# Kernel tuning notes

Hardware: AMD Instinct MI355X
Metric: run time of the kernel (lower is better)

Reference implementation:

```python
import jax, jax.numpy as jnp
import numpy as np

N_NODES = 100000
N_EDGES = 1600000
N_FEAT = 500
N_CLASSES = 40


def gcn_conv(x, W, b, src, dst, n):
    """PyG GCNConv: add self-loops, symmetric deg normalization, linear + bias."""
    h = x @ W                                   # [n, out]
    loop = jnp.arange(n, dtype=src.dtype)
    s = jnp.concatenate([src, loop])            # sources incl. self-loops
    d = jnp.concatenate([dst, loop])            # destinations incl. self-loops
    deg = jax.ops.segment_sum(jnp.ones_like(d, dtype=x.dtype), d, num_segments=n)
    dinv = jax.lax.rsqrt(deg)                   # deg >= 1 because of self-loops
    norm = dinv[s] * dinv[d]                    # [E+n]
    out = jax.ops.segment_sum(h[s] * norm[:, None], d, num_segments=n)
    return out + b


def glorot(key, fan_in, fan_out):
    lim = np.sqrt(6.0 / (fan_in + fan_out)).astype(np.float32)
    return jax.random.uniform(key, (fan_in, fan_out), jnp.float32, -lim, lim)


def setup_inputs() -> dict:
    key = jax.random.key(0)
    ks = jax.random.split(key, 6)
    x = jax.random.normal(ks[0], (N_NODES, N_FEAT), dtype=jnp.float32)
    edge_index = jax.random.randint(ks[1], (2, N_EDGES), 0, N_NODES, dtype=jnp.int64)
    return {
        "x": x,
        "edge_index": edge_index,
        "W1": glorot(ks[2], N_FEAT, 128), "b1": jnp.zeros((128,), jnp.float32),
        "W2": glorot(ks[3], 128, 64),     "b2": jnp.zeros((64,), jnp.float32),
        "W4": glorot(ks[4], 64, N_CLASSES), "b4": jnp.zeros((N_CLASSES,), jnp.float32),
    }


def reference(x, edge_index, W1, b1, W2, b2, W4, b4):
    src, dst = edge_index[0], edge_index[1]
    n = x.shape[0]
    h = jax.nn.relu(gcn_conv(x, W1, b1, src, dst, n))
    h = jax.nn.relu(gcn_conv(h, W2, b2, src, dst, n))
    h = gcn_conv(h, W4, b4, src, dst, n)
    return jax.nn.log_softmax(h, axis=1)
```

## Files before the change

kernel.cpp:

```cpp
#include <hip/hip_runtime.h>
#include <hip/hip_bf16.h>
#include <cmath>

#define NNODES 100000
#define NEDGES 1600000
#define SCAN_B 1024

typedef __attribute__((ext_vector_type(8))) short bf16x8;
typedef __attribute__((ext_vector_type(4))) float f32x4;

__device__ __forceinline__ unsigned short f2bf(float f) {
    unsigned u = __builtin_bit_cast(unsigned, f);
    unsigned r = (u + 0x7fffu + ((u >> 16) & 1u)) >> 16;
    return (unsigned short)r;
}
__device__ __forceinline__ float bflo(unsigned v) {
    return __builtin_bit_cast(float, v << 16);
}
__device__ __forceinline__ float bfhi(unsigned v) {
    return __builtin_bit_cast(float, v & 0xffff0000u);
}


__global__ void zero_deg(int* __restrict__ deg, int n) {
    int i = blockIdx.x * 256 + threadIdx.x;
    if (i < n) deg[i] = 0;
}

__global__ __launch_bounds__(256) void count_deg_xcd(const int* __restrict__ dst,
                                                     int* __restrict__ deg, int E) {
    int g = blockIdx.x & 7;
    int sub = blockIdx.x >> 3;
    int nsub = gridDim.x >> 3;
    int lo = g * (NNODES / 8), hi = lo + (NNODES / 8);
    for (int e = sub * 256 + threadIdx.x; e < E; e += nsub * 256) {
        int d = dst[e];
        if (d >= lo && d < hi) atomicAdd(&deg[d], 1);
    }
}

__global__ void calc_dinv(const int* __restrict__ deg, float* __restrict__ dinv, int n) {
    int i = blockIdx.x * 256 + threadIdx.x;
    if (i < n) dinv[i] = rsqrtf(1.0f + (float)deg[i]);
}

__global__ __launch_bounds__(SCAN_B) void scan_block(const int* __restrict__ deg,
                                                     int* __restrict__ pos,
                                                     int* __restrict__ bsums, int n) {
    __shared__ int s[SCAN_B];
    int tid = threadIdx.x;
    int gid = blockIdx.x * SCAN_B + tid;
    int v = (gid < n) ? deg[gid] : 0;
    s[tid] = v;
    __syncthreads();
    for (int off = 1; off < SCAN_B; off <<= 1) {
        int t = (tid >= off) ? s[tid - off] : 0;
        __syncthreads();
        s[tid] += t;
        __syncthreads();
    }
    if (gid < n) pos[gid] = s[tid] - v;
    if (tid == SCAN_B - 1) bsums[blockIdx.x] = s[tid];
}

__global__ __launch_bounds__(128) void scan_sums(int* __restrict__ bsums, int nb) {
    __shared__ int s[128];
    int tid = threadIdx.x;
    int v = (tid < nb) ? bsums[tid] : 0;
    s[tid] = v;
    __syncthreads();
    for (int off = 1; off < 128; off <<= 1) {
        int t = (tid >= off) ? s[tid - off] : 0;
        __syncthreads();
        s[tid] += t;
        __syncthreads();
    }
    if (tid < nb) bsums[tid] = s[tid] - v;
}

__global__ __launch_bounds__(SCAN_B) void add_off(int* __restrict__ pos,
                                                  const int* __restrict__ bsums, int n) {
    int gid = blockIdx.x * SCAN_B + threadIdx.x;
    if (gid < n) pos[gid] += bsums[blockIdx.x];
}

__global__ __launch_bounds__(256) void csr_fill_xcd(const int* __restrict__ src,
                                                    const int* __restrict__ dst,
                                                    int* __restrict__ pos,
                                                    int* __restrict__ csr_src, int E) {
    int g = blockIdx.x & 7;
    int sub = blockIdx.x >> 3;
    int nsub = gridDim.x >> 3;
    int lo = g * (NNODES / 8), hi = lo + (NNODES / 8);
    for (int e = sub * 256 + threadIdx.x; e < E; e += nsub * 256) {
        int d = dst[e];
        if (d >= lo && d < hi) {
            int slot = atomicAdd(&pos[d], 1);
            csr_src[slot] = src[e];
        }
    }
}


__global__ __launch_bounds__(256) void conv_w1f(const float* __restrict__ W1,
                                                unsigned short* __restrict__ W1f) {
    int idx = blockIdx.x * 256 + threadIdx.x;
    if (idx >= 8192) return;
    int t = idx >> 9;
    int rest = idx & 511;
    int j = rest >> 6;
    int l = rest & 63;
    int n = j * 16 + (l & 15);
    int kb = t * 32 + (l >> 4) * 8;
    bf16x8 o;
    #pragma unroll
    for (int jj = 0; jj < 8; jj++) {
        int k = kb + jj;
        o[jj] = (k < 500) ? (short)f2bf(W1[k * 128 + n]) : (short)0;
    }
    *(bf16x8*)(W1f + (size_t)idx * 8) = o;
}

__global__ __launch_bounds__(256) void conv_w2f(const float* __restrict__ W2,
                                                unsigned short* __restrict__ W2f) {
    int idx = blockIdx.x * 256 + threadIdx.x;
    if (idx >= 1024) return;
    int t = idx >> 8;
    int rest = idx & 255;
    int j = rest >> 6;
    int l = rest & 63;
    int n = j * 16 + (l & 15);
    int kb = t * 32 + (l >> 4) * 8;
    bf16x8 o;
    #pragma unroll
    for (int jj = 0; jj < 8; jj++)
        o[jj] = (short)f2bf(W2[(kb + jj) * 64 + n]);
    *(bf16x8*)(W2f + (size_t)idx * 8) = o;
}


__global__ __launch_bounds__(256) void gemm1_mfma(
    const float* __restrict__ x, const unsigned short* __restrict__ W1f,
    const float* __restrict__ dinv, unsigned short* __restrict__ C, int M)
{
    const int tid = threadIdx.x;
    const int w = tid >> 6;
    const int l = tid & 63;
    const int lm = l & 15;
    const int q = l >> 4;
    const int row0 = blockIdx.x * 128;

    const float* abase[2];
    #pragma unroll
    for (int i = 0; i < 2; i++) {
        int r = row0 + w * 32 + i * 16 + lm;
        if (r >= M) r = M - 1;
        abase[i] = x + (size_t)r * 500 + q * 8;
    }

    f32x4 acc[2][8];
    #pragma unroll
    for (int i = 0; i < 2; i++)
        #pragma unroll
        for (int j = 0; j < 8; j++) acc[i][j] = (f32x4){0.f, 0.f, 0.f, 0.f};

    for (int t = 0; t < 16; ++t) {
        const int k0 = t * 32;
        bf16x8 af[2];
        if (k0 + q * 8 + 8 <= 500) {
            #pragma unroll
            for (int i = 0; i < 2; i++) {
                float4 u = *(const float4*)(abase[i] + k0);
                float4 v = *(const float4*)(abase[i] + k0 + 4);
                bf16x8 o;
                o[0] = f2bf(u.x); o[1] = f2bf(u.y); o[2] = f2bf(u.z); o[3] = f2bf(u.w);
                o[4] = f2bf(v.x); o[5] = f2bf(v.y); o[6] = f2bf(v.z); o[7] = f2bf(v.w);
                af[i] = o;
            }
        } else {
            #pragma unroll
            for (int i = 0; i < 2; i++) {
                bf16x8 o;
                #pragma unroll
                for (int jj = 0; jj < 8; jj++) {
                    int k = k0 + q * 8 + jj;
                    o[jj] = (k < 500) ? (short)f2bf(abase[i][k0 + jj]) : (short)0;
                }
                af[i] = o;
            }
        }
        bf16x8 bfr[8];
        #pragma unroll
        for (int j = 0; j < 8; j++)
            bfr[j] = *(const bf16x8*)(W1f + (((size_t)t * 8 + j) * 64 + l) * 8);
        #pragma unroll
        for (int i = 0; i < 2; i++)
            #pragma unroll
            for (int j = 0; j < 8; j++)
                acc[i][j] = __builtin_amdgcn_mfma_f32_16x16x32_bf16(af[i], bfr[j], acc[i][j], 0, 0, 0);
    }

    #pragma unroll
    for (int i = 0; i < 2; i++) {
        #pragma unroll
        for (int reg = 0; reg < 4; reg++) {
            int grow = row0 + w * 32 + i * 16 + q * 4 + reg;
            if (grow < M) {
                float d = dinv[grow];
                #pragma unroll
                for (int j = 0; j < 8; j++)
                    C[(size_t)grow * 128 + j * 16 + lm] = f2bf(d * acc[i][j][reg]);
            }
        }
    }
}


__global__ __launch_bounds__(256) void gemm2_mfma(
    const unsigned short* __restrict__ A, const unsigned short* __restrict__ W2f,
    const float* __restrict__ dinv, unsigned short* __restrict__ C, int M)
{
    const int tid = threadIdx.x;
    const int w = tid >> 6;
    const int l = tid & 63;
    const int lm = l & 15;
    const int q = l >> 4;
    const int row0 = blockIdx.x * 128;

    const unsigned short* abase[2];
    #pragma unroll
    for (int i = 0; i < 2; i++) {
        int r = row0 + w * 32 + i * 16 + lm;
        if (r >= M) r = M - 1;
        abase[i] = A + (size_t)r * 128 + q * 8;
    }

    f32x4 acc[2][4];
    #pragma unroll
    for (int i = 0; i < 2; i++)
        #pragma unroll
        for (int j = 0; j < 4; j++) acc[i][j] = (f32x4){0.f, 0.f, 0.f, 0.f};

    for (int t = 0; t < 4; ++t) {
        const int k0 = t * 32;
        bf16x8 af[2];
        #pragma unroll
        for (int i = 0; i < 2; i++)
            af[i] = *(const bf16x8*)(abase[i] + k0);
        bf16x8 bfr[4];
        #pragma unroll
        for (int j = 0; j < 4; j++)
            bfr[j] = *(const bf16x8*)(W2f + (((size_t)t * 4 + j) * 64 + l) * 8);
        #pragma unroll
        for (int i = 0; i < 2; i++)
            #pragma unroll
            for (int j = 0; j < 4; j++)
                acc[i][j] = __builtin_amdgcn_mfma_f32_16x16x32_bf16(af[i], bfr[j], acc[i][j], 0, 0, 0);
    }

    #pragma unroll
    for (int i = 0; i < 2; i++) {
        #pragma unroll
        for (int reg = 0; reg < 4; reg++) {
            int grow = row0 + w * 32 + i * 16 + q * 4 + reg;
            if (grow < M) {
                float d = dinv[grow];
                #pragma unroll
                for (int j = 0; j < 4; j++)
                    C[(size_t)grow * 64 + j * 16 + lm] = f2bf(d * acc[i][j][reg]);
            }
        }
    }
}


__global__ __launch_bounds__(256) void gemm_n40(
    const float* __restrict__ A, const float* __restrict__ W,
    const float* __restrict__ bias, const float* __restrict__ dinv,
    float* __restrict__ C, int M)
{
    __shared__ float sA[32][65];
    __shared__ float sW[64][40];
    const int row0 = blockIdx.x * 32;
    for (int idx = threadIdx.x; idx < 64 * 40; idx += 256)
        sW[idx / 40][idx % 40] = W[idx];
    for (int idx = threadIdx.x; idx < 32 * 64; idx += 256) {
        int r = idx >> 6, k = idx & 63;
        int row = row0 + r;
        float v = 0.0f;
        if (row < M) v = fmaxf(A[(long)row * 64 + k] + bias[k], 0.0f);
        sA[r][k] = v;
    }
    __syncthreads();
    float acc[5] = {0, 0, 0, 0, 0};
    int rr[5], cc[5];
    #pragma unroll
    for (int j = 0; j < 5; j++) {
        int o = threadIdx.x + 256 * j;
        rr[j] = o / 40; cc[j] = o % 40;
    }
    for (int k = 0; k < 64; k++) {
        #pragma unroll
        for (int j = 0; j < 5; j++) acc[j] += sA[rr[j]][k] * sW[k][cc[j]];
    }
    #pragma unroll
    for (int j = 0; j < 5; j++) {
        int row = row0 + rr[j];
        if (row < M) C[(long)row * 40 + cc[j]] = dinv[row] * acc[j];
    }
}


template<int F, bool OBF16>
__global__ __launch_bounds__(256) void gather_bf(
    const unsigned short* __restrict__ h, const float* __restrict__ dinv,
    const int* __restrict__ pos, const int* __restrict__ csr_src,
    void* __restrict__ outv, const float* __restrict__ bias, int n)
{
    constexpr int P = F / 2;
    unsigned t = blockIdx.x * 256u + threadIdx.x;
    unsigned node = t / P;
    unsigned p = t - node * P;
    if (node >= (unsigned)n) return;
    int e0 = node ? pos[node - 1] : 0;
    int e1 = pos[node];
    float di = dinv[node];
    unsigned sv = *(const unsigned*)(h + (size_t)node * F + 2 * p);
    float a0 = bflo(sv);
    float a1 = bfhi(sv);
    int j = e0;
    for (; j + 4 <= e1; j += 4) {
        int s0 = csr_src[j], s1 = csr_src[j + 1], s2 = csr_src[j + 2], s3 = csr_src[j + 3];
        unsigned v0 = *(const unsigned*)(h + (size_t)s0 * F + 2 * p);
        unsigned v1 = *(const unsigned*)(h + (size_t)s1 * F + 2 * p);
        unsigned v2 = *(const unsigned*)(h + (size_t)s2 * F + 2 * p);
        unsigned v3 = *(const unsigned*)(h + (size_t)s3 * F + 2 * p);
        a0 += bflo(v0) + bflo(v1) + bflo(v2) + bflo(v3);
        a1 += bfhi(v0) + bfhi(v1) + bfhi(v2) + bfhi(v3);
    }
    for (; j < e1; j++) {
        int s = csr_src[j];
        unsigned v = *(const unsigned*)(h + (size_t)s * F + 2 * p);
        a0 += bflo(v);
        a1 += bfhi(v);
    }
    a0 *= di; a1 *= di;
    if constexpr (OBF16) {
        a0 = fmaxf(a0 + bias[2 * p], 0.0f);
        a1 = fmaxf(a1 + bias[2 * p + 1], 0.0f);
        ((unsigned*)outv)[(size_t)node * P + p] =
            ((unsigned)f2bf(a1) << 16) | (unsigned)f2bf(a0);
    } else {
        float2 r; r.x = a0; r.y = a1;
        ((float2*)outv)[(size_t)node * P + p] = r;
    }
}


template<int F>
__global__ __launch_bounds__(256) void gather_agg(
    const float* __restrict__ h, const float* __restrict__ dinv,
    const int* __restrict__ pos, const int* __restrict__ csr_src,
    float* __restrict__ out, int n)
{
    unsigned t = blockIdx.x * 256u + threadIdx.x;
    unsigned node = t / F;
    unsigned c = t - node * F;
    if (node >= (unsigned)n) return;
    int e0 = node ? pos[node - 1] : 0;
    int e1 = pos[node];
    float di = dinv[node];
    float acc = h[(size_t)node * F + c];
    int j = e0;
    for (; j + 4 <= e1; j += 4) {
        int s0 = csr_src[j], s1 = csr_src[j + 1], s2 = csr_src[j + 2], s3 = csr_src[j + 3];
        float v0 = h[(size_t)s0 * F + c];
        float v1 = h[(size_t)s1 * F + c];
        float v2 = h[(size_t)s2 * F + c];
        float v3 = h[(size_t)s3 * F + c];
        acc += v0 + v1 + v2 + v3;
    }
    for (; j < e1; j++) {
        int s = csr_src[j];
        acc += h[(size_t)s * F + c];
    }
    out[(size_t)node * F + c] = di * acc;
}


__global__ __launch_bounds__(256) void logsoftmax40(const float* __restrict__ h,
                                                    const float* __restrict__ bias,
                                                    float* __restrict__ out, int n) {
    int wave = (blockIdx.x * 256 + threadIdx.x) >> 6;
    int lane = threadIdx.x & 63;
    if (wave >= n) return;
    float x = 0.0f, v = -INFINITY;
    if (lane < 40) { x = h[(long)wave * 40 + lane] + bias[lane]; v = x; }
    #pragma unroll
    for (int off = 32; off; off >>= 1) v = fmaxf(v, __shfl_xor(v, off, 64));
    float ex = (lane < 40) ? expf(x - v) : 0.0f;
    float s = ex;
    #pragma unroll
    for (int off = 32; off; off >>= 1) s += __shfl_xor(s, off, 64);
    if (lane < 40) out[(long)wave * 40 + lane] = x - v - logf(s);
}


extern "C" void kernel_launch(void* const* d_in, const int* in_sizes, int n_in,
                              void* d_out, int out_size, void* d_ws, size_t ws_size,
                              hipStream_t stream) {
    const float* x  = (const float*)d_in[0];
    const int*   ei = (const int*)d_in[1];
    const float* W1 = (const float*)d_in[2];
    const float* b1 = (const float*)d_in[3];
    const float* W2 = (const float*)d_in[4];
    const float* b2 = (const float*)d_in[5];
    const float* W4 = (const float*)d_in[6];
    const float* b4 = (const float*)d_in[7];
    float* out = (float*)d_out;
    float* ws  = (float*)d_ws;

    const int N = NNODES, E = NEDGES;
    const int* src = ei;
    const int* dst = ei + E;

    float*          dinv    = ws;
    int*            deg     = (int*)(ws + 100000);
    int*            pos     = (int*)(ws + 200000);
    int*            bsums   = (int*)(ws + 300000);
    int*            csr_src = (int*)(ws + 300200);
    unsigned short* W1f     = (unsigned short*)(ws + 1900200);
    unsigned short* W2f     = (unsigned short*)(ws + 1933000);
    unsigned short* h1      = (unsigned short*)(ws + 1937100);
    unsigned short* h2      = (unsigned short*)(ws + 1937100);
    unsigned short* a1      = (unsigned short*)(ws + 8337100);
    float*          h3      = ws + 8337100;
    float*          a2      = ws + 14737100;
    float*          a3      = out;

    const int nscan = (N + SCAN_B - 1) / SCAN_B;

    zero_deg<<<(N + 255) / 256, 256, 0, stream>>>(deg, N);
    count_deg_xcd<<<1024, 256, 0, stream>>>(dst, deg, E);
    calc_dinv<<<(N + 255) / 256, 256, 0, stream>>>(deg, dinv, N);
    scan_block<<<nscan, SCAN_B, 0, stream>>>(deg, pos, bsums, N);
    scan_sums<<<1, 128, 0, stream>>>(bsums, nscan);
    add_off<<<nscan, SCAN_B, 0, stream>>>(pos, bsums, N);
    csr_fill_xcd<<<1024, 256, 0, stream>>>(src, dst, pos, csr_src, E);

    conv_w1f<<<32, 256, 0, stream>>>(W1, W1f);
    conv_w2f<<<4, 256, 0, stream>>>(W2, W2f);

    gemm1_mfma<<<(N + 127) / 128, 256, 0, stream>>>(x, W1f, dinv, h1, N);
    {
        unsigned tot = (unsigned)N * 64u;
        gather_bf<128, true><<<(tot + 255) / 256, 256, 0, stream>>>(h1, dinv, pos, csr_src, a1, b1, N);
    }

    gemm2_mfma<<<(N + 127) / 128, 256, 0, stream>>>(a1, W2f, dinv, h2, N);
    {
        unsigned tot = (unsigned)N * 32u;
        gather_bf<64, false><<<(tot + 255) / 256, 256, 0, stream>>>(h2, dinv, pos, csr_src, a2, nullptr, N);
    }

    gemm_n40<<<(N + 31) / 32, 256, 0, stream>>>(a2, W4, b2, dinv, h3, N);
    {
        unsigned tot = (unsigned)N * 40u;
        gather_agg<40><<<(tot + 255) / 256, 256, 0, stream>>>(h3, dinv, pos, csr_src, a3, N);
    }

    logsoftmax40<<<(N * 64 + 255) / 256, 256, 0, stream>>>(a3, b4, out, N);
}
```

Before: 764.3 us.

## Software-pipeline gemm1 loads with double-buffered fragments and halve rows per block

Rewrites the first GEMM so each wave computes 16 rows instead of 32, and blocks cover 64 rows, doubling the grid. Within the K loop, A and B fragments for the next k-step are loaded into a second register buffer while MFMAs run on the current one, hiding global load latency. The cost is more B-fragment reloads per output row, since W1 is read once per 16 rows rather than per 32, while fewer accumulators may improve occupancy.

```diff
diff --git a/kernel.cpp b/kernel.cpp
--- a/kernel.cpp
+++ b/kernel.cpp
@@ -138,6 +138,23 @@
     *(bf16x8*)(W2f + (size_t)idx * 8) = o;
 }
 
+__device__ __forceinline__ bf16x8 load_a_frag(const float* __restrict__ abase, int k0, int q) {
+    bf16x8 o;
+    if (k0 + q * 8 + 8 <= 500) {
+        float4 u = *(const float4*)(abase + k0);
+        float4 v = *(const float4*)(abase + k0 + 4);
+        o[0] = f2bf(u.x); o[1] = f2bf(u.y); o[2] = f2bf(u.z); o[3] = f2bf(u.w);
+        o[4] = f2bf(v.x); o[5] = f2bf(v.y); o[6] = f2bf(v.z); o[7] = f2bf(v.w);
+    } else {
+        #pragma unroll
+        for (int jj = 0; jj < 8; jj++) {
+            int k = k0 + q * 8 + jj;
+            o[jj] = (k < 500) ? (short)f2bf(abase[k0 + jj]) : (short)0;
+        }
+    }
+    return o;
+}
+
 
 __global__ __launch_bounds__(256) void gemm1_mfma(
     const float* __restrict__ x, const unsigned short* __restrict__ W1f,
@@ -148,69 +165,52 @@
     const int l = tid & 63;
     const int lm = l & 15;
     const int q = l >> 4;
-    const int row0 = blockIdx.x * 128;
-
-    const float* abase[2];
-    #pragma unroll
-    for (int i = 0; i < 2; i++) {
-        int r = row0 + w * 32 + i * 16 + lm;
-        if (r >= M) r = M - 1;
-        abase[i] = x + (size_t)r * 500 + q * 8;
-    }
-
-    f32x4 acc[2][8];
-    #pragma unroll
-    for (int i = 0; i < 2; i++)
-        #pragma unroll
-        for (int j = 0; j < 8; j++) acc[i][j] = (f32x4){0.f, 0.f, 0.f, 0.f};
-
-    for (int t = 0; t < 16; ++t) {
-        const int k0 = t * 32;
-        bf16x8 af[2];
-        if (k0 + q * 8 + 8 <= 500) {
-            #pragma unroll
-            for (int i = 0; i < 2; i++) {
-                float4 u = *(const float4*)(abase[i] + k0);
-                float4 v = *(const float4*)(abase[i] + k0 + 4);
-                bf16x8 o;
-                o[0] = f2bf(u.x); o[1] = f2bf(u.y); o[2] = f2bf(u.z); o[3] = f2bf(u.w);
-                o[4] = f2bf(v.x); o[5] = f2bf(v.y); o[6] = f2bf(v.z); o[7] = f2bf(v.w);
-                af[i] = o;
-            }
-        } else {
-            #pragma unroll
-            for (int i = 0; i < 2; i++) {
-                bf16x8 o;
-                #pragma unroll
-                for (int jj = 0; jj < 8; jj++) {
-                    int k = k0 + q * 8 + jj;
-                    o[jj] = (k < 500) ? (short)f2bf(abase[i][k0 + jj]) : (short)0;
-                }
-                af[i] = o;
-            }
-        }
-        bf16x8 bfr[8];
+    const int row0 = blockIdx.x * 64;
+
+    int r = row0 + w * 16 + lm;
+    if (r >= M) r = M - 1;
+    const float* abase = x + (size_t)r * 500 + q * 8;
+    const unsigned short* bbase = W1f + (size_t)l * 8;
+
+    f32x4 acc[8];
+    #pragma unroll
+    for (int j = 0; j < 8; j++) acc[j] = (f32x4){0.f, 0.f, 0.f, 0.f};
+
+    bf16x8 a0, a1, b0[8], b1[8];
+
+    a0 = load_a_frag(abase, 0, q);
+    #pragma unroll
+    for (int j = 0; j < 8; j++)
+        b0[j] = *(const bf16x8*)(bbase + (size_t)j * 512);
+
+    for (int tt = 0; tt < 8; ++tt) {
+        const int t0 = 2 * tt, t1 = 2 * tt + 1;
+        a1 = load_a_frag(abase, t1 * 32, q);
         #pragma unroll
         for (int j = 0; j < 8; j++)
-            bfr[j] = *(const bf16x8*)(W1f + (((size_t)t * 8 + j) * 64 + l) * 8);
-        #pragma unroll
-        for (int i = 0; i < 2; i++)
+            b1[j] = *(const bf16x8*)(bbase + (size_t)(t1 * 8 + j) * 512);
+        #pragma unroll
+        for (int j = 0; j < 8; j++)
+            acc[j] = __builtin_amdgcn_mfma_f32_16x16x32_bf16(a0, b0[j], acc[j], 0, 0, 0);
+        if (t0 + 2 < 16) {
+            a0 = load_a_frag(abase, (t0 + 2) * 32, q);
             #pragma unroll
             for (int j = 0; j < 8; j++)
-                acc[i][j] = __builtin_amdgcn_mfma_f32_16x16x32_bf16(af[i], bfr[j], acc[i][j], 0, 0, 0);
-    }
-
-    #pragma unroll
-    for (int i = 0; i < 2; i++) {
-        #pragma unroll
-        for (int reg = 0; reg < 4; reg++) {
-            int grow = row0 + w * 32 + i * 16 + q * 4 + reg;
-            if (grow < M) {
-                float d = dinv[grow];
-                #pragma unroll
-                for (int j = 0; j < 8; j++)
-                    C[(size_t)grow * 128 + j * 16 + lm] = f2bf(d * acc[i][j][reg]);
-            }
+                b0[j] = *(const bf16x8*)(bbase + (size_t)((t0 + 2) * 8 + j) * 512);
+        }
+        #pragma unroll
+        for (int j = 0; j < 8; j++)
+            acc[j] = __builtin_amdgcn_mfma_f32_16x16x32_bf16(a1, b1[j], acc[j], 0, 0, 0);
+    }
+
+    #pragma unroll
+    for (int reg = 0; reg < 4; reg++) {
+        int grow = row0 + w * 16 + q * 4 + reg;
+        if (grow < M) {
+            float d = dinv[grow];
+            #pragma unroll
+            for (int j = 0; j < 8; j++)
+                C[(size_t)grow * 128 + j * 16 + lm] = f2bf(d * acc[j][reg]);
         }
     }
 }
@@ -451,7 +451,7 @@
     conv_w1f<<<32, 256, 0, stream>>>(W1, W1f);
     conv_w2f<<<4, 256, 0, stream>>>(W2, W2f);
 
-    gemm1_mfma<<<(N + 127) / 128, 256, 0, stream>>>(x, W1f, dinv, h1, N);
+    gemm1_mfma<<<(N + 63) / 64, 256, 0, stream>>>(x, W1f, dinv, h1, N);
     {
         unsigned tot = (unsigned)N * 64u;
         gather_bf<128, true><<<(tot + 255) / 256, 256, 0, stream>>>(h1, dinv, pos, csr_src, a1, b1, N);
```

New measurement: 765.4 us. About the same (+0.1%).
